# Kernel optimization log

Hardware: AMD Instinct MI355X
Metric: run time of the kernel (lower is better)

The kernel has to match this reference:

```python
import jax, jax.numpy as jnp
import numpy as np
import math

N = 50000        # nodes
E = 800000       # edges (avg degree 16)
F_IN = 128
F_OUT = 64


def setup_inputs() -> dict:
    key = jax.random.key(0)
    k = jax.random.split(key, 7)
    stdv = 1.0 / math.sqrt(F_OUT)
    x = jax.random.normal(k[0], (N, F_IN), dtype=jnp.float32)
    t = jax.random.uniform(k[1], (N,), dtype=jnp.float32)
    src = jax.random.randint(k[2], (E,), 0, N, dtype=jnp.int64)
    dst = jax.random.randint(k[3], (E,), 0, N, dtype=jnp.int64)
    # sparse adjacency values (e.g. normalized adjacency weights)
    edge_vals = jax.random.uniform(k[4], (E,), dtype=jnp.float32)
    weight = jax.random.uniform(k[5], (F_IN, F_OUT), dtype=jnp.float32,
                                minval=-stdv, maxval=stdv)
    bias = jax.random.uniform(k[6], (F_OUT,), dtype=jnp.float32,
                              minval=-stdv, maxval=stdv)
    return {"x": x, "t": t, "src": src, "dst": dst,
            "edge_vals": edge_vals, "weight": weight, "bias": bias}


def reference(x, t, src, dst, edge_vals, weight, bias):
    # support = (X @ W) * t[:, None]   -- dense GEMM + per-row scale
    support = (x @ weight) * t[:, None]                 # [N, F_OUT]
    # spmm(adj, support): gather rows at src, scale by edge value, reduce by dst
    msgs = support[src] * edge_vals[:, None]            # [E, F_OUT]
    out = jax.ops.segment_sum(msgs, dst, num_segments=N)  # [N, F_OUT]
    return out + bias
```

## Files before the change

### kernel.cpp

```cpp
#include <hip/hip_runtime.h>
#include <hip/hip_bf16.h>

#define FIN 128
#define FOUT 64
#define TILE_ROWS 64

#define EPB 2048
#define NPB 64
#define NBUK_MAX 800
#define CAP 1408

#define OFF_CUR   6400000
#define OFF_OVFC  6403200
#define OFF_TMP   6403264
#define OFF_OVF   15414464

typedef short bf16x8 __attribute__((ext_vector_type(8)));
typedef float f32x4  __attribute__((ext_vector_type(4)));

__device__ inline ushort f32_to_bf16_rne(float f) {
    unsigned u = __float_as_uint(f);
    u += 0x7FFFu + ((u >> 16) & 1u);
    return (ushort)(u >> 16);
}
__device__ inline float bf16_to_f32(ushort h) {
    return __uint_as_float((unsigned)h << 16);
}

union __align__(16) K1Sh {
    ushort wt[FOUT * FIN];
    struct { int h[NBUK_MAX]; int c[NBUK_MAX]; } sc;
};

__global__ __launch_bounds__(256) void gemm_scatter_kernel(
    const float* __restrict__ x, const float* __restrict__ t,
    const float* __restrict__ W, ushort* __restrict__ support, int N,
    const int* __restrict__ src, const int* __restrict__ dst,
    const float* __restrict__ ev, int* __restrict__ cur,
    int2* __restrict__ tmp, int* __restrict__ ovfc, int4* __restrict__ ovf,
    int E, int SBP, int NBUK, int GB)
{
    __shared__ K1Sh sh;
    const int tid = threadIdx.x;

    if (blockIdx.x >= (unsigned)GB) {
        const int chunk = blockIdx.x - GB;
        const int e0    = chunk * EPB;

        for (int i = tid; i < NBUK; i += 256) sh.sc.h[i] = 0;
        __syncthreads();

        for (int i = tid; i < EPB; i += 256) {
            int e = e0 + i;
            if (e < E) atomicAdd(&sh.sc.h[dst[e] >> 6], 1);
        }
        __syncthreads();

        for (int j = tid; j < NBUK; j += 256) {
            int hj = sh.sc.h[j];
            if (hj) sh.sc.c[j] = atomicAdd(&cur[j], hj);
        }
        __syncthreads();

        for (int i = tid; i < EPB; i += 256) {
            int e = e0 + i;
            if (e < E) {
                int d = dst[e];
                int j = d >> 6;
                int s = atomicAdd(&sh.sc.c[j], 1);
                int2 rec = make_int2(src[e] | ((d & (NPB - 1)) << 16),
                                     __float_as_int(ev[e]));
                if (s < CAP) {
                    tmp[(size_t)j * CAP + s] = rec;
                } else {
                    int o = atomicAdd(ovfc, 1);
                    if (o < E) ovf[o] = make_int4(rec.x, rec.y, j, 0);
                }
            }
        }
        return;
    }

    const int gb   = blockIdx.x;
    const int lane = tid & 63;
    const int w    = tid >> 6;
    const int ln   = lane & 15;
    const int q    = lane >> 4;
    const int rowb = gb * TILE_ROWS + w * 16;
    const int arow = rowb + ln;

    for (int idx = tid; idx < FIN * FOUT; idx += 256) {
        int k = idx >> 6;
        int n = idx & 63;
        sh.wt[n * FIN + (k ^ ((n & 7) << 3))] = f32_to_bf16_rne(W[idx]);
    }
    __syncthreads();

    f32x4 acc[4];
    #pragma unroll
    for (int nt = 0; nt < 4; ++nt)
        #pragma unroll
        for (int r = 0; r < 4; ++r) acc[nt][r] = 0.f;

    const bool aok = (arow < N);
    const float* xrow = &x[(size_t)arow * FIN];

    #pragma unroll
    for (int kc = 0; kc < 4; ++kc) {
        float xs[8];
        #pragma unroll
        for (int j = 0; j < 8; ++j) xs[j] = 0.f;
        if (aok) {
            float4 x0 = *(const float4*)&xrow[kc * 32 + q * 8];
            float4 x1 = *(const float4*)&xrow[kc * 32 + q * 8 + 4];
            xs[0] = x0.x; xs[1] = x0.y; xs[2] = x0.z; xs[3] = x0.w;
            xs[4] = x1.x; xs[5] = x1.y; xs[6] = x1.z; xs[7] = x1.w;
        }
        bf16x8 a;
        #pragma unroll
        for (int j = 0; j < 8; ++j) a[j] = (short)f32_to_bf16_rne(xs[j]);

        const int k0 = kc * 32 + q * 8;
        #pragma unroll
        for (int nt = 0; nt < 4; ++nt) {
            bf16x8 b = *(const bf16x8*)
                &sh.wt[(nt * 16 + ln) * FIN + (k0 ^ ((ln & 7) << 3))];
            acc[nt] = __builtin_amdgcn_mfma_f32_16x16x32_bf16(a, b, acc[nt], 0, 0, 0);
        }
    }

    #pragma unroll
    for (int reg = 0; reg < 4; ++reg) {
        int r = rowb + q * 4 + reg;
        if (r < N) {
            float tv = t[r];
            #pragma unroll
            for (int nt = 0; nt < 4; ++nt)
                support[(size_t)r * FOUT + nt * 16 + ln] =
                    f32_to_bf16_rne(acc[nt][reg] * tv);
        }
    }
}

__global__ __launch_bounds__(256) void bucket_gather_kernel(
    const int* __restrict__ curg, const int2* __restrict__ tmp,
    const ushort* __restrict__ support, const float* __restrict__ bias,
    float* __restrict__ out, const int* __restrict__ ovfc,
    const int4* __restrict__ ovf, int E, int N, int NBUK)
{
    __shared__ int2 raw[CAP];
    __shared__ int2 sorted[CAP];
    __shared__ int  cnt[NPB];
    __shared__ int  starts[NPB + 1];
    __shared__ int  cur[NPB];
    __shared__ int  novs;

    const int tid   = threadIdx.x;
    const int w     = tid >> 6;
    const int lane  = tid & 63;
    const int B     = blockIdx.x;
    const int node0 = B * NPB;

    const int base   = B * CAP;
    const int tot    = curg[B];
    const int placed = (tot < CAP) ? tot : CAP;

    if (tid < NPB) cnt[tid] = 0;
    __syncthreads();

    for (int i = tid; i < placed; i += 256) {
        int2 r = tmp[base + i];
        raw[i] = r;
        atomicAdd(&cnt[(r.x >> 16) & (NPB - 1)], 1);
    }
    __syncthreads();

    if (tid < 64) {
        int v   = cnt[tid];
        int val = v;
        #pragma unroll
        for (int d = 1; d < NPB; d <<= 1) {
            int n = __shfl_up(val, d);
            if (tid >= d) val += n;
        }
        starts[tid] = val - v;
        cur[tid]    = val - v;
        if (tid == 0) starts[NPB] = placed;
    }
    __syncthreads();

    for (int i = tid; i < placed; i += 256) {
        int2 r  = raw[i];
        int pos = atomicAdd(&cur[(r.x >> 16) & (NPB - 1)], 1);
        sorted[pos] = r;
    }
    __syncthreads();

    const float bv = bias[lane];
    const int rbeg = starts[w * 16];
    const int rend = starts[w * 16 + 16];

    float accv = 0.f;
    int   curn = -1;

    int i = rbeg;
    while (i + 8 <= rend) {
        int2 r[8];
        #pragma unroll
        for (int u = 0; u < 8; ++u) r[u] = sorted[i + u];
        float v[8];
        #pragma unroll
        for (int u = 0; u < 8; ++u)
            v[u] = bf16_to_f32(support[(size_t)(r[u].x & 0xFFFF) * FOUT + lane]);
        #pragma unroll
        for (int u = 0; u < 8; ++u) {
            int n = (r[u].x >> 16) & (NPB - 1);
            if (n != curn) {
                if (curn >= 0 && node0 + curn < N)
                    out[(size_t)(node0 + curn) * FOUT + lane] = accv + bv;
                curn = n;
                accv = 0.f;
            }
            accv += v[u] * __int_as_float(r[u].y);
        }
        i += 8;
    }
    while (i < rend) {
        int2 a = sorted[i];
        float va = bf16_to_f32(support[(size_t)(a.x & 0xFFFF) * FOUT + lane]);
        int n = (a.x >> 16) & (NPB - 1);
        if (n != curn) {
            if (curn >= 0 && node0 + curn < N)
                out[(size_t)(node0 + curn) * FOUT + lane] = accv + bv;
            curn = n;
            accv = 0.f;
        }
        accv += va * __int_as_float(a.y);
        ++i;
    }
    if (curn >= 0 && node0 + curn < N)
        out[(size_t)(node0 + curn) * FOUT + lane] = accv + bv;

    for (int n = w; n < NPB; n += 4) {
        int node = node0 + n;
        if (node < N && cnt[n] == 0)
            out[(size_t)node * FOUT + lane] = bv;
    }

    __syncthreads();
    if (tid == 0) novs = *ovfc;
    __syncthreads();
    int nov = novs;
    if (nov > 0) {
        if (nov > E) nov = E;
        __threadfence();
        for (int k = w; k < nov; k += 4) {
            int4 r = ovf[k];
            if (r.z == B) {
                int node = node0 + ((r.x >> 16) & (NPB - 1));
                if (node < N) {
                    float v = bf16_to_f32(
                        support[(size_t)(r.x & 0xFFFF) * FOUT + lane]);
                    atomicAdd(&out[(size_t)node * FOUT + lane],
                              v * __int_as_float(r.y));
                }
            }
        }
    }
}

extern "C" void kernel_launch(void* const* d_in, const int* in_sizes, int n_in,
                              void* d_out, int out_size, void* d_ws, size_t ws_size,
                              hipStream_t stream) {
    const float* x    = (const float*)d_in[0];
    const float* t    = (const float*)d_in[1];
    const int*   src  = (const int*)d_in[2];
    const int*   dst  = (const int*)d_in[3];
    const float* ev   = (const float*)d_in[4];
    const float* W    = (const float*)d_in[5];
    const float* bias = (const float*)d_in[6];
    float* out = (float*)d_out;

    const int N = in_sizes[1];
    const int E = in_sizes[2];

    char*   ws      = (char*)d_ws;
    ushort* support = (ushort*)ws;
    int*    cur     = (int*)(ws + OFF_CUR);
    int*    ovfc    = (int*)(ws + OFF_OVFC);
    int2*   tmp     = (int2*)(ws + OFF_TMP);
    int4*   ovf     = (int4*)(ws + OFF_OVF);

    const int GB   = (N + TILE_ROWS - 1) / TILE_ROWS;
    const int SBP  = (E + EPB - 1) / EPB;
    const int NBUK = (N + NPB - 1) / NPB;

    hipMemsetAsync(ws + OFF_CUR, 0, OFF_TMP - OFF_CUR, stream);

    gemm_scatter_kernel<<<GB + SBP, 256, 0, stream>>>(
        x, t, W, support, N, src, dst, ev, cur, tmp, ovfc, ovf,
        E, SBP, NBUK, GB);

    bucket_gather_kernel<<<NBUK, 256, 0, stream>>>(
        cur, tmp, support, bias, out, ovfc, ovf, E, N, NBUK);
}
```

Measured before the change: 141.7 us.

## Split each node's edges across four lane groups with vectorized bf16 gathers

Replaces the per-lane sequential edge walk, where each lane owned one output feature, with a per-node loop. Four 16-lane groups each take every fourth edge and load four bf16 features per lane as one uint2, then combine partials with xor shuffles and store one float4. The aim is wider memory transactions and more gathers in flight, at the cost of shuffle reductions, a fixed 16-node loop per wave and idle lanes on low-degree nodes. EPB also goes from 2048 to 8192, which changes the edge partitioning per block.

Measured after the change: 153.8 us. 1.09x slower.

```diff
diff --git a/kernel.cpp b/kernel.cpp
--- a/kernel.cpp
+++ b/kernel.cpp
@@ -5,7 +5,7 @@
 #define FOUT 64
 #define TILE_ROWS 64
 
-#define EPB 2048
+#define EPB 8192
 #define NPB 64
 #define NBUK_MAX 800
 #define CAP 1408
@@ -196,55 +196,40 @@
     }
     __syncthreads();
 
-    const float bv = bias[lane];
-    const int rbeg = starts[w * 16];
-    const int rend = starts[w * 16 + 16];
-
-    float accv = 0.f;
-    int   curn = -1;
-
-    int i = rbeg;
-    while (i + 8 <= rend) {
-        int2 r[8];
-        #pragma unroll
-        for (int u = 0; u < 8; ++u) r[u] = sorted[i + u];
-        float v[8];
-        #pragma unroll
-        for (int u = 0; u < 8; ++u)
-            v[u] = bf16_to_f32(support[(size_t)(r[u].x & 0xFFFF) * FOUT + lane]);
-        #pragma unroll
-        for (int u = 0; u < 8; ++u) {
-            int n = (r[u].x >> 16) & (NPB - 1);
-            if (n != curn) {
-                if (curn >= 0 && node0 + curn < N)
-                    out[(size_t)(node0 + curn) * FOUT + lane] = accv + bv;
-                curn = n;
-                accv = 0.f;
-            }
-            accv += v[u] * __int_as_float(r[u].y);
-        }
-        i += 8;
-    }
-    while (i < rend) {
-        int2 a = sorted[i];
-        float va = bf16_to_f32(support[(size_t)(a.x & 0xFFFF) * FOUT + lane]);
-        int n = (a.x >> 16) & (NPB - 1);
-        if (n != curn) {
-            if (curn >= 0 && node0 + curn < N)
-                out[(size_t)(node0 + curn) * FOUT + lane] = accv + bv;
-            curn = n;
-            accv = 0.f;
-        }
-        accv += va * __int_as_float(a.y);
-        ++i;
-    }
-    if (curn >= 0 && node0 + curn < N)
-        out[(size_t)(node0 + curn) * FOUT + lane] = accv + bv;
-
-    for (int n = w; n < NPB; n += 4) {
-        int node = node0 + n;
-        if (node < N && cnt[n] == 0)
-            out[(size_t)node * FOUT + lane] = bv;
+    const int fl = lane & 15;
+    const int g  = lane >> 4;
+    const float4 bv4 = *(const float4*)&bias[fl * 4];
+
+    for (int nn = 0; nn < 16; ++nn) {
+        const int nl = w * 16 + nn;
+        const int rb = starts[nl];
+        const int re = starts[nl + 1];
+
+        float a0 = 0.f, a1 = 0.f, a2 = 0.f, a3 = 0.f;
+        for (int i = rb + g; i < re; i += 4) {
+            int2 r = sorted[i];
+            uint2 u = *(const uint2*)
+                &support[(size_t)(r.x & 0xFFFF) * FOUT + fl * 4];
+            float wg = __int_as_float(r.y);
+            a0 += bf16_to_f32((ushort)(u.x & 0xFFFFu)) * wg;
+            a1 += bf16_to_f32((ushort)(u.x >> 16)) * wg;
+            a2 += bf16_to_f32((ushort)(u.y & 0xFFFFu)) * wg;
+            a3 += bf16_to_f32((ushort)(u.y >> 16)) * wg;
+        }
+        #pragma unroll
+        for (int d = 16; d < 64; d <<= 1) {
+            a0 += __shfl_xor(a0, d);
+            a1 += __shfl_xor(a1, d);
+            a2 += __shfl_xor(a2, d);
+            a3 += __shfl_xor(a3, d);
+        }
+        const int node = node0 + nl;
+        if (g == 0 && node < N) {
+            float4 o;
+            o.x = a0 + bv4.x; o.y = a1 + bv4.y;
+            o.z = a2 + bv4.z; o.w = a3 + bv4.w;
+            *(float4*)&out[(size_t)node * FOUT + fl * 4] = o;
+        }
     }
 
     __syncthreads();
```
